# Kernel tuning notes

Hardware: AMD Instinct MI355X
Metric: run time of the kernel (lower is better)

The kernel has to match this reference:

```python
import jax, jax.numpy as jnp
import numpy as np


def setup_inputs() -> dict:
    key = jax.random.key(0)
    k = jax.random.split(key, 5)
    B, S, D, H = 4, 2048, 2048, 8192
    scale1 = 1.0 / np.sqrt(D)
    scale2 = 1.0 / np.sqrt(H)
    return {
        "x": jax.random.normal(k[0], (B, S, D), dtype=jnp.float32),
        "w1": jax.random.normal(k[1], (H, D), dtype=jnp.float32) * scale1,
        "b1": jax.random.normal(k[2], (H,), dtype=jnp.float32) * scale1,
        "w2": jax.random.normal(k[3], (D, H), dtype=jnp.float32) * scale2,
        "b2": jax.random.normal(k[4], (D,), dtype=jnp.float32) * scale2,
    }


def reference(x, w1, b1, w2, b2):
    # fc1: [B,S,D] @ [D,H] -> [B,S,H]
    h = jnp.einsum("bsd,hd->bsh", x, w1) + b1
    # squared ReLU activation
    a = jnp.square(jax.nn.relu(h))
    # fc2: [B,S,H] @ [H,D] -> [B,S,D]
    return jnp.einsum("bsh,dh->bsd", a, w2) + b2
```

## Files before the change

kernel.cpp:

```cpp
#include <hip/hip_runtime.h>
#include <hip/hip_bf16.h>
#include <stdint.h>

typedef __bf16 bf16x8 __attribute__((ext_vector_type(8)));
typedef float f32x4 __attribute__((ext_vector_type(4)));


__device__ inline void gload_lds16(const void* g, void* lds) {
  __builtin_amdgcn_global_load_lds(
      (const __attribute__((address_space(1))) uint32_t*)(uintptr_t)g,
      (__attribute__((address_space(3))) uint32_t*)(uintptr_t)lds,
      16, 0, 0);
}

__device__ inline bf16x8 ds_readv(uint32_t addr) {
  bf16x8 r;
  asm volatile("ds_read_b128 %0, %1" : "=v"(r) : "v"(addr));
  return r;
}

#define LGKM(N) do {                                             \
    asm volatile("s_waitcnt lgkmcnt(" #N ")" ::: "memory");      \
    __builtin_amdgcn_sched_barrier(0);                           \
  } while (0)

__device__ inline short f2bf(float f) {
  union { float f; uint32_t u; } x; x.f = f;
  uint32_t u = x.u;
  u += 0x7fffu + ((u >> 16) & 1u);
  return (short)(u >> 16);
}

#define BAR() do { asm volatile("" ::: "memory"); \
                   __builtin_amdgcn_s_barrier();  \
                   asm volatile("" ::: "memory"); } while (0)


__global__ __launch_bounds__(256) void cvt_f32_bf16(
    const float* __restrict__ in, short* __restrict__ out, int n4) {
  int i = blockIdx.x * 256 + threadIdx.x;
  if (i < n4) {
    float4 v = reinterpret_cast<const float4*>(in)[i];
    short4 o;
    o.x = f2bf(v.x); o.y = f2bf(v.y); o.z = f2bf(v.z); o.w = f2bf(v.w);
    reinterpret_cast<short4*>(out)[i] = o;
  }
}


template <int EPI>
__global__ __launch_bounds__(512, 2) void gemm_bt(
    const short* __restrict__ A, const short* __restrict__ B,
    const float* __restrict__ bias, void* __restrict__ Cout,
    int M, int N, int K) {
  __shared__ __align__(16) short lds[2][4][128 * 64];

  const int tid  = threadIdx.x;
  const int wave = tid >> 6;
  const int lane = tid & 63;
  const int wr = wave >> 2;
  const int wc = wave & 3;
  const int fr = lane & 15, kq = lane >> 4;

  const int nwg = gridDim.x;
  const int w = (blockIdx.x & 7) * (nwg >> 3) + (blockIdx.x >> 3);
  const int gy = M >> 8;
  const int brow = w % gy;
  const int bcol = w / gy;

  f32x4 acc[8][4];
#pragma unroll
  for (int m = 0; m < 8; ++m)
#pragma unroll
    for (int n = 0; n < 4; ++n)
      acc[m][n] = (f32x4){0.f, 0.f, 0.f, 0.f};

  const int nk = K >> 6;

  const uint32_t LB = (uint32_t)(uintptr_t)&lds[0][0][0];
  uint32_t aA[4][2], aB[2][2];
#pragma unroll
  for (int m = 0; m < 4; ++m)
#pragma unroll
    for (int kk = 0; kk < 2; ++kk) {
      int r = wr * 64 + m * 16 + fr;
      int g = r * 8 + kk * 4 + kq;
      aA[m][kk] = LB + (uint32_t)((g ^ (r & 7)) * 16);
    }
#pragma unroll
  for (int n = 0; n < 2; ++n)
#pragma unroll
    for (int kk = 0; kk < 2; ++kk) {
      int r = wc * 32 + n * 16 + fr;
      int g = r * 8 + kk * 4 + kq;
      aB[n][kk] = LB + (uint32_t)((g ^ (r & 7)) * 16);
    }

  const int i0 = tid;
  const int gl0 = i0 ^ ((i0 >> 3) & 7);
  const int r0 = gl0 >> 3, c0 = gl0 & 7;
  const size_t rstep = (size_t)128 * K;

  const short* pA[2];
  const short* pB[2];
  {
    const int rb0 = (r0 >> 5) * 64 + (r0 & 31);
#pragma unroll
    for (int h = 0; h < 2; ++h) {
      pA[h] = A + (size_t)(brow * 256 + h * 64 + r0) * K + c0 * 8;
      pB[h] = B + (size_t)(bcol * 256 + rb0 + h * 32) * K + c0 * 8;
    }
  }

  const int dst0 = wave * 512, dst1 = 4096 + wave * 512;

#define STAGE(p, buf, slot)                              \
  do {                                                   \
    short* base_ = &lds[buf][slot][0];                   \
    gload_lds16((p), base_ + dst0);                      \
    gload_lds16((p) + rstep, base_ + dst1);              \
    (p) += 64;                                           \
  } while (0)

  STAGE(pA[0], 0, 0);
  STAGE(pA[1], 0, 1);
  STAGE(pB[0], 0, 2);
  STAGE(pB[1], 0, 3);
  asm volatile("s_waitcnt vmcnt(0)" ::: "memory");
  BAR();

  for (int t = 0; t < nk; ++t) {
    const int cur = t & 1, nxt = cur ^ 1;
    const bool s1 = (t + 1) < nk;

    if (s1) {
      STAGE(pA[0], nxt, 0);
      STAGE(pA[1], nxt, 1);
      STAGE(pB[0], nxt, 2);
      STAGE(pB[1], nxt, 3);
    }

    const uint32_t cb = (uint32_t)cur << 16;

    bf16x8 bq0[2][2], a0q[4][2], a1q[4][2], bq1[2][2];
#pragma unroll
    for (int n = 0; n < 2; ++n)
#pragma unroll
      for (int kk = 0; kk < 2; ++kk)
        bq0[n][kk] = ds_readv(aB[n][kk] + cb + 32768u);
#pragma unroll
    for (int m = 0; m < 4; ++m)
#pragma unroll
      for (int kk = 0; kk < 2; ++kk)
        a0q[m][kk] = ds_readv(aA[m][kk] + cb);
#pragma unroll
    for (int m = 0; m < 4; ++m)
#pragma unroll
      for (int kk = 0; kk < 2; ++kk)
        a1q[m][kk] = ds_readv(aA[m][kk] + cb + 16384u);
#pragma unroll
    for (int n = 0; n < 2; ++n)
#pragma unroll
      for (int kk = 0; kk < 2; ++kk)
        bq1[n][kk] = ds_readv(aB[n][kk] + cb + 49152u);

    LGKM(12);
    __builtin_amdgcn_s_setprio(1);
#pragma unroll
    for (int m = 0; m < 4; ++m)
#pragma unroll
      for (int n = 0; n < 2; ++n)
#pragma unroll
        for (int kk = 0; kk < 2; ++kk)
          acc[m][n] = __builtin_amdgcn_mfma_f32_16x16x32_bf16(
              bq0[n][kk], a0q[m][kk], acc[m][n], 0, 0, 0);
    __builtin_amdgcn_s_setprio(0);

    LGKM(4);
    __builtin_amdgcn_s_setprio(1);
#pragma unroll
    for (int m = 0; m < 4; ++m)
#pragma unroll
      for (int n = 0; n < 2; ++n)
#pragma unroll
        for (int kk = 0; kk < 2; ++kk)
          acc[m + 4][n] = __builtin_amdgcn_mfma_f32_16x16x32_bf16(
              bq0[n][kk], a1q[m][kk], acc[m + 4][n], 0, 0, 0);
    __builtin_amdgcn_s_setprio(0);

    LGKM(0);
    __builtin_amdgcn_s_setprio(1);
#pragma unroll
    for (int m = 0; m < 4; ++m)
#pragma unroll
      for (int n = 0; n < 2; ++n)
#pragma unroll
        for (int kk = 0; kk < 2; ++kk)
          acc[m + 4][n + 2] = __builtin_amdgcn_mfma_f32_16x16x32_bf16(
              bq1[n][kk], a1q[m][kk], acc[m + 4][n + 2], 0, 0, 0);
    __builtin_amdgcn_s_setprio(0);
    __builtin_amdgcn_s_setprio(1);
#pragma unroll
    for (int m = 0; m < 4; ++m)
#pragma unroll
      for (int n = 0; n < 2; ++n)
#pragma unroll
        for (int kk = 0; kk < 2; ++kk)
          acc[m][n + 2] = __builtin_amdgcn_mfma_f32_16x16x32_bf16(
              bq1[n][kk], a0q[m][kk], acc[m][n + 2], 0, 0, 0);
    __builtin_amdgcn_s_setprio(0);

    if (s1) {
      asm volatile("s_waitcnt vmcnt(0)" ::: "memory");
      BAR();
    }
  }

  const int q = lane >> 4;
  if (EPI == 0) {
    short* C = (short*)Cout;
#pragma unroll
    for (int m = 0; m < 8; ++m) {
      const int row = brow * 256 + wr * 128 + m * 16 + fr;
#pragma unroll
      for (int n = 0; n < 4; ++n) {
        const int col = bcol * 256 + wc * 64 + n * 16 + q * 4;
        const float4 bv = *(const float4*)&bias[col];
        short4 o;
        float v0 = acc[m][n][0] + bv.x; v0 = v0 > 0.f ? v0 * v0 : 0.f;
        float v1 = acc[m][n][1] + bv.y; v1 = v1 > 0.f ? v1 * v1 : 0.f;
        float v2 = acc[m][n][2] + bv.z; v2 = v2 > 0.f ? v2 * v2 : 0.f;
        float v3 = acc[m][n][3] + bv.w; v3 = v3 > 0.f ? v3 * v3 : 0.f;
        o.x = f2bf(v0); o.y = f2bf(v1); o.z = f2bf(v2); o.w = f2bf(v3);
        *(short4*)&C[(size_t)row * N + col] = o;
      }
    }
  } else {
    float* C = (float*)Cout;
#pragma unroll
    for (int m = 0; m < 8; ++m) {
      const int row = brow * 256 + wr * 128 + m * 16 + fr;
#pragma unroll
      for (int n = 0; n < 4; ++n) {
        const int col = bcol * 256 + wc * 64 + n * 16 + q * 4;
        const float4 bv = *(const float4*)&bias[col];
        float4 o;
        o.x = acc[m][n][0] + bv.x;
        o.y = acc[m][n][1] + bv.y;
        o.z = acc[m][n][2] + bv.z;
        o.w = acc[m][n][3] + bv.w;
        *(float4*)&C[(size_t)row * N + col] = o;
      }
    }
  }
#undef STAGE
}


extern "C" void kernel_launch(void* const* d_in, const int* in_sizes, int n_in,
                              void* d_out, int out_size, void* d_ws,
                              size_t ws_size, hipStream_t stream) {
  const float* x  = (const float*)d_in[0];
  const float* w1 = (const float*)d_in[1];
  const float* b1 = (const float*)d_in[2];
  const float* w2 = (const float*)d_in[3];
  const float* b2 = (const float*)d_in[4];
  float* out = (float*)d_out;

  const int H = in_sizes[2];
  const int D = in_sizes[4];
  const int M = in_sizes[0] / D;

  short* xb  = (short*)d_ws;
  short* w1b = xb  + (size_t)M * D;
  short* w2b = w1b + (size_t)H * D;
  short* act = w2b + (size_t)D * H;

  {
    int n4 = (M * D) / 4;
    cvt_f32_bf16<<<(n4 + 255) / 256, 256, 0, stream>>>(x, xb, n4);
    n4 = (H * D) / 4;
    cvt_f32_bf16<<<(n4 + 255) / 256, 256, 0, stream>>>(w1, w1b, n4);
    n4 = (D * H) / 4;
    cvt_f32_bf16<<<(n4 + 255) / 256, 256, 0, stream>>>(w2, w2b, n4);
  }

  gemm_bt<0><<<(M / 256) * (H / 256), 512, 0, stream>>>(
      xb, w1b, b1, (void*)act, M, H, D);
  gemm_bt<1><<<(M / 256) * (D / 256), 512, 0, stream>>>(
      act, w2b, b2, (void*)out, M, D, H);
}
```

Measured before the change: 572.7 us.

## Load B fragments directly from global into registers, bypassing LDS

The B operand no longer goes through LDS. Each wave loads its B fragments straight into registers with global_load_dwordx4, double-buffered across iterations, and the loop is unrolled by two with ping-pong register sets. Only the A tile stays in LDS, which halves LDS use and the ds_read traffic per iteration. The costs are more register pressure, B data duplicated across the two wave rows, and less coalesced global access for B. The loop also assumes the k-tile count is even.

```diff
diff --git a/kernel.cpp b/kernel.cpp
--- a/kernel.cpp
+++ b/kernel.cpp
@@ -19,8 +19,16 @@
   return r;
 }
 
+#define GLB(dst, p, OFF)                                            \
+  asm volatile("global_load_dwordx4 %0, %1, off offset:" #OFF       \
+               : "=v"(dst) : "v"(p))
+
 #define LGKM(N) do {                                             \
     asm volatile("s_waitcnt lgkmcnt(" #N ")" ::: "memory");      \
+    __builtin_amdgcn_sched_barrier(0);                           \
+  } while (0)
+#define VM(N) do {                                               \
+    asm volatile("s_waitcnt vmcnt(" #N ")" ::: "memory");        \
     __builtin_amdgcn_sched_barrier(0);                           \
   } while (0)
 
@@ -53,7 +61,7 @@
     const short* __restrict__ A, const short* __restrict__ B,
     const float* __restrict__ bias, void* __restrict__ Cout,
     int M, int N, int K) {
-  __shared__ __align__(16) short lds[2][4][128 * 64];
+  __shared__ __align__(16) short lds[2][2][128 * 64];
 
   const int tid  = threadIdx.x;
   const int wave = tid >> 6;
@@ -78,7 +86,7 @@
   const int nk = K >> 6;
 
   const uint32_t LB = (uint32_t)(uintptr_t)&lds[0][0][0];
-  uint32_t aA[4][2], aB[2][2];
+  uint32_t aA[4][2];
 #pragma unroll
   for (int m = 0; m < 4; ++m)
 #pragma unroll
@@ -87,14 +95,6 @@
       int g = r * 8 + kk * 4 + kq;
       aA[m][kk] = LB + (uint32_t)((g ^ (r & 7)) * 16);
     }
-#pragma unroll
-  for (int n = 0; n < 2; ++n)
-#pragma unroll
-    for (int kk = 0; kk < 2; ++kk) {
-      int r = wc * 32 + n * 16 + fr;
-      int g = r * 8 + kk * 4 + kq;
-      aB[n][kk] = LB + (uint32_t)((g ^ (r & 7)) * 16);
-    }
 
   const int i0 = tid;
   const int gl0 = i0 ^ ((i0 >> 3) & 7);
@@ -102,15 +102,14 @@
   const size_t rstep = (size_t)128 * K;
 
   const short* pA[2];
-  const short* pB[2];
-  {
-    const int rb0 = (r0 >> 5) * 64 + (r0 & 31);
-#pragma unroll
-    for (int h = 0; h < 2; ++h) {
-      pA[h] = A + (size_t)(brow * 256 + h * 64 + r0) * K + c0 * 8;
-      pB[h] = B + (size_t)(bcol * 256 + rb0 + h * 32) * K + c0 * 8;
-    }
-  }
+#pragma unroll
+  for (int h = 0; h < 2; ++h)
+    pA[h] = A + (size_t)(brow * 256 + h * 64 + r0) * K + c0 * 8;
+
+  const short* pBF[4];
+#pragma unroll
+  for (int n = 0; n < 4; ++n)
+    pBF[n] = B + (size_t)(bcol * 256 + wc * 64 + n * 16 + fr) * K + kq * 8;
 
   const int dst0 = wave * 512, dst1 = 4096 + wave * 512;
 
@@ -122,98 +121,101 @@
     (p) += 64;                                           \
   } while (0)
 
+  bf16x8 a0q[4][2], a1q[4][2];
+  bf16x8 bqX[4][2], bqY[4][2];
+
+  auto BFRAG = [&](bf16x8 (&bs)[4][2]) {
+    GLB(bs[0][0], pBF[0], 0);  GLB(bs[0][1], pBF[0], 64);
+    GLB(bs[1][0], pBF[1], 0);  GLB(bs[1][1], pBF[1], 64);
+    GLB(bs[2][0], pBF[2], 0);  GLB(bs[2][1], pBF[2], 64);
+    GLB(bs[3][0], pBF[3], 0);  GLB(bs[3][1], pBF[3], 64);
+    pBF[0] += 64; pBF[1] += 64; pBF[2] += 64; pBF[3] += 64;
+  };
+  auto RD_A0 = [&](uint32_t cb) {
+#pragma unroll
+    for (int m = 0; m < 4; ++m)
+#pragma unroll
+      for (int kk = 0; kk < 2; ++kk)
+        a0q[m][kk] = ds_readv(aA[m][kk] + cb);
+  };
+  auto RD_A1 = [&](uint32_t cb) {
+#pragma unroll
+    for (int m = 0; m < 4; ++m)
+#pragma unroll
+      for (int kk = 0; kk < 2; ++kk)
+        a1q[m][kk] = ds_readv(aA[m][kk] + cb + 16384u);
+  };
+  auto Q1 = [&](bf16x8 (&bs)[4][2]) {
+#pragma unroll
+    for (int m = 0; m < 4; ++m)
+#pragma unroll
+      for (int n = 0; n < 2; ++n)
+#pragma unroll
+        for (int kk = 0; kk < 2; ++kk)
+          acc[m][n] = __builtin_amdgcn_mfma_f32_16x16x32_bf16(
+              bs[n][kk], a0q[m][kk], acc[m][n], 0, 0, 0);
+  };
+  auto Q2 = [&](bf16x8 (&bs)[4][2]) {
+#pragma unroll
+    for (int m = 0; m < 4; ++m)
+#pragma unroll
+      for (int n = 0; n < 2; ++n)
+#pragma unroll
+        for (int kk = 0; kk < 2; ++kk)
+          acc[m][n + 2] = __builtin_amdgcn_mfma_f32_16x16x32_bf16(
+              bs[n + 2][kk], a0q[m][kk], acc[m][n + 2], 0, 0, 0);
+  };
+  auto Q3 = [&](bf16x8 (&bs)[4][2]) {
+#pragma unroll
+    for (int m = 0; m < 4; ++m)
+#pragma unroll
+      for (int n = 0; n < 2; ++n)
+#pragma unroll
+        for (int kk = 0; kk < 2; ++kk)
+          acc[m + 4][n + 2] = __builtin_amdgcn_mfma_f32_16x16x32_bf16(
+              bs[n + 2][kk], a1q[m][kk], acc[m + 4][n + 2], 0, 0, 0);
+  };
+  auto Q4 = [&](bf16x8 (&bs)[4][2]) {
+#pragma unroll
+    for (int m = 0; m < 4; ++m)
+#pragma unroll
+      for (int n = 0; n < 2; ++n)
+#pragma unroll
+        for (int kk = 0; kk < 2; ++kk)
+          acc[m + 4][n] = __builtin_amdgcn_mfma_f32_16x16x32_bf16(
+              bs[n][kk], a1q[m][kk], acc[m + 4][n], 0, 0, 0);
+  };
+
+#define PRIO_ON  __builtin_amdgcn_s_setprio(1)
+#define PRIO_OFF __builtin_amdgcn_s_setprio(0)
+
+  auto body = [&](int t, uint32_t cb, int nxt,
+                  bf16x8 (&bqC)[4][2], bf16x8 (&bqN)[4][2]) {
+    const bool s1 = (t + 1) < nk;
+    RD_A0(cb);
+    if (s1) { STAGE(pA[0], nxt, 0); STAGE(pA[1], nxt, 1); }
+    __builtin_amdgcn_sched_barrier(0);
+    if (s1) BFRAG(bqN);
+    if (s1) { VM(12); } else { VM(0); }
+    LGKM(0);
+    PRIO_ON; Q1(bqC); PRIO_OFF;
+    RD_A1(cb);
+    PRIO_ON; Q2(bqC); PRIO_OFF;
+    LGKM(0);
+    PRIO_ON; Q3(bqC); Q4(bqC); PRIO_OFF;
+    if (s1) { VM(8); BAR(); }
+  };
+
   STAGE(pA[0], 0, 0);
   STAGE(pA[1], 0, 1);
-  STAGE(pB[0], 0, 2);
-  STAGE(pB[1], 0, 3);
-  asm volatile("s_waitcnt vmcnt(0)" ::: "memory");
+  __builtin_amdgcn_sched_barrier(0);
+  BFRAG(bqX);
+  VM(8);
   BAR();
 
-  for (int t = 0; t < nk; ++t) {
-    const int cur = t & 1, nxt = cur ^ 1;
-    const bool s1 = (t + 1) < nk;
-
-    if (s1) {
-      STAGE(pA[0], nxt, 0);
-      STAGE(pA[1], nxt, 1);
-      STAGE(pB[0], nxt, 2);
-      STAGE(pB[1], nxt, 3);
-    }
-
-    const uint32_t cb = (uint32_t)cur << 16;
-
-    bf16x8 bq0[2][2], a0q[4][2], a1q[4][2], bq1[2][2];
-#pragma unroll
-    for (int n = 0; n < 2; ++n)
-#pragma unroll
-      for (int kk = 0; kk < 2; ++kk)
-        bq0[n][kk] = ds_readv(aB[n][kk] + cb + 32768u);
-#pragma unroll
-    for (int m = 0; m < 4; ++m)
-#pragma unroll
-      for (int kk = 0; kk < 2; ++kk)
-        a0q[m][kk] = ds_readv(aA[m][kk] + cb);
-#pragma unroll
-    for (int m = 0; m < 4; ++m)
-#pragma unroll
-      for (int kk = 0; kk < 2; ++kk)
-        a1q[m][kk] = ds_readv(aA[m][kk] + cb + 16384u);
-#pragma unroll
-    for (int n = 0; n < 2; ++n)
-#pragma unroll
-      for (int kk = 0; kk < 2; ++kk)
-        bq1[n][kk] = ds_readv(aB[n][kk] + cb + 49152u);
-
-    LGKM(12);
-    __builtin_amdgcn_s_setprio(1);
-#pragma unroll
-    for (int m = 0; m < 4; ++m)
-#pragma unroll
-      for (int n = 0; n < 2; ++n)
-#pragma unroll
-        for (int kk = 0; kk < 2; ++kk)
-          acc[m][n] = __builtin_amdgcn_mfma_f32_16x16x32_bf16(
-              bq0[n][kk], a0q[m][kk], acc[m][n], 0, 0, 0);
-    __builtin_amdgcn_s_setprio(0);
-
-    LGKM(4);
-    __builtin_amdgcn_s_setprio(1);
-#pragma unroll
-    for (int m = 0; m < 4; ++m)
-#pragma unroll
-      for (int n = 0; n < 2; ++n)
-#pragma unroll
-        for (int kk = 0; kk < 2; ++kk)
-          acc[m + 4][n] = __builtin_amdgcn_mfma_f32_16x16x32_bf16(
-              bq0[n][kk], a1q[m][kk], acc[m + 4][n], 0, 0, 0);
-    __builtin_amdgcn_s_setprio(0);
-
-    LGKM(0);
-    __builtin_amdgcn_s_setprio(1);
-#pragma unroll
-    for (int m = 0; m < 4; ++m)
-#pragma unroll
-      for (int n = 0; n < 2; ++n)
-#pragma unroll
-        for (int kk = 0; kk < 2; ++kk)
-          acc[m + 4][n + 2] = __builtin_amdgcn_mfma_f32_16x16x32_bf16(
-              bq1[n][kk], a1q[m][kk], acc[m + 4][n + 2], 0, 0, 0);
-    __builtin_amdgcn_s_setprio(0);
-    __builtin_amdgcn_s_setprio(1);
-#pragma unroll
-    for (int m = 0; m < 4; ++m)
-#pragma unroll
-      for (int n = 0; n < 2; ++n)
-#pragma unroll
-        for (int kk = 0; kk < 2; ++kk)
-          acc[m][n + 2] = __builtin_amdgcn_mfma_f32_16x16x32_bf16(
-              bq1[n][kk], a0q[m][kk], acc[m][n + 2], 0, 0, 0);
-    __builtin_amdgcn_s_setprio(0);
-
-    if (s1) {
-      asm volatile("s_waitcnt vmcnt(0)" ::: "memory");
-      BAR();
-    }
+  for (int t = 0; t < nk; t += 2) {
+    body(t,     0u,      1, bqX, bqY);
+    body(t + 1, 32768u,  0, bqY, bqX);
   }
 
   const int q = lane >> 4;
```

After: 1.768 ms. +208.7%, slower.
